# Kernel tuning notes

Hardware: AMD Instinct MI355X
Metric: run time of the kernel (lower is better)

Reference implementation:

```python
import jax, jax.numpy as jnp
import numpy as np
from jax import lax

B, T, F = 2048, 512, 8
C = 16   # conv out channels
H = 10   # lstm hidden size


def setup_inputs() -> dict:
    key = jax.random.key(0)
    ks = jax.random.split(key, 12)
    s_conv = 1.0 / np.sqrt(F * 3)
    s1 = 1.0 / np.sqrt(H)
    inp = {
        'x': jax.random.normal(ks[0], (B, T, F), dtype=jnp.float32),
        'conv_w': jax.random.uniform(ks[1], (C, F, 3), jnp.float32, -s_conv, s_conv),
        'conv_b': jax.random.uniform(ks[2], (C,), jnp.float32, -s_conv, s_conv),
        'w_ih1': jax.random.uniform(ks[3], (4 * H, C), jnp.float32, -s1, s1),
        'w_hh1': jax.random.uniform(ks[4], (4 * H, H), jnp.float32, -s1, s1),
        'b_ih1': jax.random.uniform(ks[5], (4 * H,), jnp.float32, -s1, s1),
        'b_hh1': jax.random.uniform(ks[6], (4 * H,), jnp.float32, -s1, s1),
        'w_ih2': jax.random.uniform(ks[7], (4 * H, H), jnp.float32, -s1, s1),
        'w_hh2': jax.random.uniform(ks[8], (4 * H, H), jnp.float32, -s1, s1),
        'b_ih2': jax.random.uniform(ks[9], (4 * H,), jnp.float32, -s1, s1),
        'b_hh2': jax.random.uniform(ks[9], (4 * H,), jnp.float32, -s1, s1),
        'lin_w': jax.random.uniform(ks[10], (1, H), jnp.float32, -s1, s1),
        'lin_b': jax.random.uniform(ks[11], (1,), jnp.float32, -s1, s1),
    }
    return inp


def _lstm(seq, w_ih, w_hh, b_ih, b_hh):
    # seq: [B, T, D] -> hidden stream [B, T, H]; PyTorch gate order i,f,g,o.
    xg = jnp.einsum('btd,gd->btg', seq, w_ih) + (b_ih + b_hh)  # [B,T,4H]
    h0 = jnp.zeros((seq.shape[0], H), seq.dtype)

    def step(carry, xg_t):
        h, c = carry
        g = xg_t + h @ w_hh.T
        i, f, gg, o = jnp.split(g, 4, axis=-1)
        c = jax.nn.sigmoid(f) * c + jax.nn.sigmoid(i) * jnp.tanh(gg)
        h = jax.nn.sigmoid(o) * jnp.tanh(c)
        return (h, c), h

    _, hs = lax.scan(step, (h0, h0), jnp.swapaxes(xg, 0, 1))  # [T,B,H]
    return jnp.swapaxes(hs, 0, 1)


def reference(x, conv_w, conv_b, w_ih1, w_hh1, b_ih1, b_hh1,
              w_ih2, w_hh2, b_ih2, b_hh2, lin_w, lin_b):
    # conv1d over time, padding=1 keeps length (dropout is identity in eval)
    xc = jnp.transpose(x, (0, 2, 1))  # [B,F,T]
    y = lax.conv_general_dilated(xc, conv_w, window_strides=(1,),
                                 padding=[(1, 1)],
                                 dimension_numbers=('NCH', 'OIH', 'NCH'))
    y = jax.nn.relu(y + conv_b[None, :, None])
    y = jnp.transpose(y, (0, 2, 1))  # [B,T,C]
    h1 = _lstm(y, w_ih1, w_hh1, b_ih1, b_hh1)
    h2 = _lstm(h1, w_ih2, w_hh2, b_ih2, b_hh2)
    last = h2[:, -1, :]  # [B,H]
    return jax.nn.sigmoid(last @ lin_w.T + lin_b)  # [B,1]
```

## Files before the change

kernel.cpp:

```cpp
#include <hip/hip_runtime.h>

#define TT 512
#define FF 8
#define CC 16
#define HH 10
#define G4 40

__device__ __forceinline__ float rl(float v, int k){
    return __int_as_float(__builtin_amdgcn_readlane(__float_as_int(v), k));
}
__device__ __forceinline__ float sigf(float z){
    return __builtin_amdgcn_rcpf(1.f + __expf(-z));
}
__device__ __forceinline__ float tanh_f(float z){
    return 1.f - 2.f * __builtin_amdgcn_rcpf(1.f + __expf(2.f * z));
}
#define PIN(v) asm volatile("" : "+v"(v))

template<int Q>
__device__ __forceinline__ float quadb(float v){
    return __int_as_float(__builtin_amdgcn_mov_dpp(__float_as_int(v), Q * 0x55, 0xf, 0xf, false));
}

#define CONV_Y(Y) do{                                                                              \
    float a0 = cb, a1 = 0.f;                                                                       \
    a0 = fmaf(w0a.x, cw0,  a0); a1 = fmaf(w1a.x, cw1,  a1); a0 = fmaf(w2a.x, cw2,  a0);            \
    a1 = fmaf(w0a.y, cw3,  a1); a0 = fmaf(w1a.y, cw4,  a0); a1 = fmaf(w2a.y, cw5,  a1);            \
    a0 = fmaf(w0a.z, cw6,  a0); a1 = fmaf(w1a.z, cw7,  a1); a0 = fmaf(w2a.z, cw8,  a0);            \
    a1 = fmaf(w0a.w, cw9,  a1); a0 = fmaf(w1a.w, cw10, a0); a1 = fmaf(w2a.w, cw11, a1);            \
    a0 = fmaf(w0b.x, cw12, a0); a1 = fmaf(w1b.x, cw13, a1); a0 = fmaf(w2b.x, cw14, a0);            \
    a1 = fmaf(w0b.y, cw15, a1); a0 = fmaf(w1b.y, cw16, a0); a1 = fmaf(w2b.y, cw17, a1);            \
    a0 = fmaf(w0b.z, cw18, a0); a1 = fmaf(w1b.z, cw19, a1); a0 = fmaf(w2b.z, cw20, a0);            \
    a1 = fmaf(w0b.w, cw21, a1); a0 = fmaf(w1b.w, cw22, a0); a1 = fmaf(w2b.w, cw23, a1);            \
    Y = fmaxf(a0 + a1, 0.f);                                                                       \
}while(0)

__global__ __launch_bounds__(64, 1)
void conv_xg(const float* __restrict__ x,
             const float* __restrict__ conv_w, const float* __restrict__ conv_b,
             const float* __restrict__ w_ih1,  const float* __restrict__ b_ih1,
             const float* __restrict__ b_hh1,
             float* __restrict__ xg)
{
    __shared__ float wl[64][43];
    const int lane = threadIdx.x;
    const int b    = blockIdx.x;
    const int ch   = lane & 15;
    const int g    = lane >> 4;
    const int u_c  = (lane < G4) ? (lane >> 2) : 9;
    const int q    = lane & 3;
    const int r    = q * 10 + u_c;

    {
        float* mr_ = wl[lane];
        const float* cwp = conv_w + ch*24;
        #pragma unroll
        for (int m = 0; m < 24; ++m) mr_[m] = cwp[m];
        const float* wip = w_ih1 + r*CC;
        #pragma unroll
        for (int k = 0; k < CC; ++k) mr_[24+k] = wip[k];
        mr_[40] = b_ih1[r] + b_hh1[r];
        mr_[41] = conv_b[ch];
    }
    __syncthreads();
    const float* mr = wl[lane];

    float cw0=mr[0],  cw1=mr[1],  cw2=mr[2],  cw3=mr[3],  cw4=mr[4],  cw5=mr[5];
    float cw6=mr[6],  cw7=mr[7],  cw8=mr[8],  cw9=mr[9],  cw10=mr[10],cw11=mr[11];
    float cw12=mr[12],cw13=mr[13],cw14=mr[14],cw15=mr[15],cw16=mr[16],cw17=mr[17];
    float cw18=mr[18],cw19=mr[19],cw20=mr[20],cw21=mr[21],cw22=mr[22],cw23=mr[23];
    PIN(cw0);PIN(cw1);PIN(cw2);PIN(cw3);PIN(cw4);PIN(cw5);PIN(cw6);PIN(cw7);
    PIN(cw8);PIN(cw9);PIN(cw10);PIN(cw11);PIN(cw12);PIN(cw13);PIN(cw14);PIN(cw15);
    PIN(cw16);PIN(cw17);PIN(cw18);PIN(cw19);PIN(cw20);PIN(cw21);PIN(cw22);PIN(cw23);
    float wi0=mr[24], wi1=mr[25], wi2=mr[26], wi3=mr[27];
    float wi4=mr[28], wi5=mr[29], wi6=mr[30], wi7=mr[31];
    float wi8=mr[32], wi9=mr[33], wi10=mr[34],wi11=mr[35];
    float wi12=mr[36],wi13=mr[37],wi14=mr[38],wi15=mr[39];
    PIN(wi0);PIN(wi1);PIN(wi2);PIN(wi3);PIN(wi4);PIN(wi5);PIN(wi6);PIN(wi7);
    PIN(wi8);PIN(wi9);PIN(wi10);PIN(wi11);PIN(wi12);PIN(wi13);PIN(wi14);PIN(wi15);
    float b1r = mr[40]; PIN(b1r);
    float cb  = mr[41]; PIN(cb);

    const float* xb  = x  + (size_t)b * (TT*FF);
    float*       xgb = xg + (size_t)b * (TT*G4);
    const float4 z4 = make_float4(0.f,0.f,0.f,0.f);

    #pragma unroll 1
    for (int tb = 0; tb < TT/4; ++tb){
        const int tq = tb*4 + g;
        float4 w0a, w0b, w1a, w1b, w2a, w2b;
        if (tq == 0){ w0a = z4; w0b = z4; }
        else { const float* p = xb + (tq-1)*FF; w0a = *(const float4*)p; w0b = *(const float4*)(p+4); }
        { const float* p = xb + tq*FF; w1a = *(const float4*)p; w1b = *(const float4*)(p+4); }
        if (tq + 1 < TT){ const float* p = xb + (tq+1)*FF; w2a = *(const float4*)p; w2b = *(const float4*)(p+4); }
        else { w2a = z4; w2b = z4; }

        float y; CONV_Y(y);

        #pragma unroll
        for (int s = 0; s < 4; ++s){
            float e0 = b1r, e1 = 0.f;
            e0 = fmaf(rl(y, s*16+0),  wi0,  e0);  e1 = fmaf(rl(y, s*16+1),  wi1,  e1);
            e0 = fmaf(rl(y, s*16+2),  wi2,  e0);  e1 = fmaf(rl(y, s*16+3),  wi3,  e1);
            e0 = fmaf(rl(y, s*16+4),  wi4,  e0);  e1 = fmaf(rl(y, s*16+5),  wi5,  e1);
            e0 = fmaf(rl(y, s*16+6),  wi6,  e0);  e1 = fmaf(rl(y, s*16+7),  wi7,  e1);
            e0 = fmaf(rl(y, s*16+8),  wi8,  e0);  e1 = fmaf(rl(y, s*16+9),  wi9,  e1);
            e0 = fmaf(rl(y, s*16+10), wi10, e0);  e1 = fmaf(rl(y, s*16+11), wi11, e1);
            e0 = fmaf(rl(y, s*16+12), wi12, e0);  e1 = fmaf(rl(y, s*16+13), wi13, e1);
            e0 = fmaf(rl(y, s*16+14), wi14, e0);  e1 = fmaf(rl(y, s*16+15), wi15, e1);
            if (lane < G4) xgb[(tb*4+s)*G4 + lane] = e0 + e1;
        }
    }
}

#define BH1B                                                                     \
    const float hs0=rl(h1,0),  hs1=rl(h1,4),  hs2=rl(h1,8),  hs3=rl(h1,12),      \
                hs4=rl(h1,16), hs5=rl(h1,20), hs6=rl(h1,24), hs7=rl(h1,28),      \
                hs8=rl(h1,32), hs9=rl(h1,36);

#define BL2 do{                                                                  \
    float d0 = b2, d1 = 0.f;                                                     \
    d0 = fmaf(hs0, wi2_0, d0);  d1 = fmaf(hs1, wi2_1, d1);                       \
    d0 = fmaf(hs2, wi2_2, d0);  d1 = fmaf(hs3, wi2_3, d1);                       \
    d0 = fmaf(hs4, wi2_4, d0);  d1 = fmaf(hs5, wi2_5, d1);                       \
    d0 = fmaf(hs6, wi2_6, d0);  d1 = fmaf(hs7, wi2_7, d1);                       \
    d0 = fmaf(hs8, wi2_8, d0);  d1 = fmaf(hs9, wi2_9, d1);                       \
    d0 = fmaf(rl(h2,0),  wh2_0, d0);  d1 = fmaf(rl(h2,4),  wh2_1, d1);           \
    d0 = fmaf(rl(h2,8),  wh2_2, d0);  d1 = fmaf(rl(h2,12), wh2_3, d1);           \
    d0 = fmaf(rl(h2,16), wh2_4, d0);  d1 = fmaf(rl(h2,20), wh2_5, d1);           \
    d0 = fmaf(rl(h2,24), wh2_6, d0);  d1 = fmaf(rl(h2,28), wh2_7, d1);           \
    d0 = fmaf(rl(h2,32), wh2_8, d0);  d1 = fmaf(rl(h2,36), wh2_9, d1);           \
    const float g2  = d0 + d1;                                                   \
    const float sg2 = sigf(g2 * zM);                                             \
    const float act2 = fmaf(aA, sg2, aB);                                        \
    const float ai2 = quadb<0>(act2);                                            \
    const float af2 = quadb<1>(act2);                                            \
    const float ag2 = quadb<2>(act2);                                            \
    const float ao2 = quadb<3>(act2);                                            \
    c2 = fmaf(af2, c2, ai2 * ag2);                                               \
    h2 = ao2 * tanh_f(c2);                                                       \
}while(0)

#define BL1(XGV) do{                                                             \
    float e0 = (XGV), e1 = 0.f;                                                  \
    e0 = fmaf(hs0, wh1_0, e0);  e1 = fmaf(hs1, wh1_1, e1);                       \
    e0 = fmaf(hs2, wh1_2, e0);  e1 = fmaf(hs3, wh1_3, e1);                       \
    e0 = fmaf(hs4, wh1_4, e0);  e1 = fmaf(hs5, wh1_5, e1);                       \
    e0 = fmaf(hs6, wh1_6, e0);  e1 = fmaf(hs7, wh1_7, e1);                       \
    e0 = fmaf(hs8, wh1_8, e0);  e1 = fmaf(hs9, wh1_9, e1);                       \
    const float g1  = e0 + e1;                                                   \
    const float sg1 = sigf(g1 * zM);                                             \
    const float act1 = fmaf(aA, sg1, aB);                                        \
    const float ai1 = quadb<0>(act1);                                            \
    const float af1 = quadb<1>(act1);                                            \
    const float ag1 = quadb<2>(act1);                                            \
    const float ao1 = quadb<3>(act1);                                            \
    c1 = fmaf(af1, c1, ai1 * ag1);                                               \
    h1n = ao1 * tanh_f(c1);                                                      \
}while(0)

__global__ __launch_bounds__(64, 1)
void lstm_seq(const float* __restrict__ xg,
              const float* __restrict__ w_hh1,
              const float* __restrict__ w_ih2,  const float* __restrict__ w_hh2,
              const float* __restrict__ b_ih2,  const float* __restrict__ b_hh2,
              const float* __restrict__ lin_w,  const float* __restrict__ lin_b,
              float* __restrict__ out)
{
    __shared__ float wl[64][31];
    const int lane  = threadIdx.x;
    const int batch = blockIdx.x;
    const int u_c   = (lane < G4) ? (lane >> 2) : 9;
    const int q     = lane & 3;
    const int r     = q * 10 + u_c;
    const bool isG  = (q == 2);
    float zM = isG ? 2.f : 1.f;
    float aA = isG ? 2.f : 1.f;
    float aB = isG ? -1.f : 0.f;
    PIN(zM); PIN(aA); PIN(aB);

    {
        float* mr_ = wl[lane];
        const float* q1 = w_hh1 + r*HH;
        const float* q2 = w_ih2 + r*HH;
        const float* q3 = w_hh2 + r*HH;
        #pragma unroll
        for (int m = 0; m < HH; ++m){ mr_[m]=q1[m]; mr_[10+m]=q2[m]; mr_[20+m]=q3[m]; }
        mr_[30] = b_ih2[r] + b_hh2[r];
    }
    __syncthreads();
    const float* mr = wl[lane];

    float wh1_0=mr[0], wh1_1=mr[1], wh1_2=mr[2], wh1_3=mr[3], wh1_4=mr[4];
    float wh1_5=mr[5], wh1_6=mr[6], wh1_7=mr[7], wh1_8=mr[8], wh1_9=mr[9];
    PIN(wh1_0);PIN(wh1_1);PIN(wh1_2);PIN(wh1_3);PIN(wh1_4);
    PIN(wh1_5);PIN(wh1_6);PIN(wh1_7);PIN(wh1_8);PIN(wh1_9);
    float wi2_0=mr[10],wi2_1=mr[11],wi2_2=mr[12],wi2_3=mr[13],wi2_4=mr[14];
    float wi2_5=mr[15],wi2_6=mr[16],wi2_7=mr[17],wi2_8=mr[18],wi2_9=mr[19];
    PIN(wi2_0);PIN(wi2_1);PIN(wi2_2);PIN(wi2_3);PIN(wi2_4);
    PIN(wi2_5);PIN(wi2_6);PIN(wi2_7);PIN(wi2_8);PIN(wi2_9);
    float wh2_0=mr[20],wh2_1=mr[21],wh2_2=mr[22],wh2_3=mr[23],wh2_4=mr[24];
    float wh2_5=mr[25],wh2_6=mr[26],wh2_7=mr[27],wh2_8=mr[28],wh2_9=mr[29];
    PIN(wh2_0);PIN(wh2_1);PIN(wh2_2);PIN(wh2_3);PIN(wh2_4);
    PIN(wh2_5);PIN(wh2_6);PIN(wh2_7);PIN(wh2_8);PIN(wh2_9);
    float b2 = mr[30]; PIN(b2);

    const float* xp = xg + (size_t)batch * (TT*G4) + ((lane < G4) ? lane : (G4-1));

    float h1 = 0.f, c1 = 0.f, h2 = 0.f, c2 = 0.f, h1n;

    float xgv = xp[0];
    {
        BH1B;
        BL1(xgv);
        h1 = h1n;
    }
    float xgn = xp[G4];

    #pragma unroll 2
    for (int t = 1; t < TT; ++t){
        const float xgc = xgn;
        const int tn = (t + 1 < TT) ? (t + 1) : (TT - 1);
        xgn = xp[(size_t)tn * G4];
        BH1B;
        BL2;
        BL1(xgc);
        h1 = h1n;
    }
    { BH1B; BL2; }

    float part = (q == 0 && lane < G4) ? h2 * lin_w[u_c] : 0.f;
    part += __shfl_xor(part, 4,  64);
    part += __shfl_xor(part, 8,  64);
    part += __shfl_xor(part, 16, 64);
    part += __shfl_xor(part, 32, 64);
    if (lane == 0) out[batch] = sigf(part + lin_b[0]);
}

#define H1BCAST                                                                                    \
    const float hs0=rl(h1,0), hs1=rl(h1,1), hs2=rl(h1,2), hs3=rl(h1,3), hs4=rl(h1,4),              \
                hs5=rl(h1,5), hs6=rl(h1,6), hs7=rl(h1,7), hs8=rl(h1,8), hs9=rl(h1,9);

#define LAYER2 do{                                                                                 \
    float d0 = b2, d1 = 0.f;                                                                       \
    d0 = fmaf(hs0, wi2_0, d0);  d1 = fmaf(hs1, wi2_1, d1);                                         \
    d0 = fmaf(hs2, wi2_2, d0);  d1 = fmaf(hs3, wi2_3, d1);                                         \
    d0 = fmaf(hs4, wi2_4, d0);  d1 = fmaf(hs5, wi2_5, d1);                                         \
    d0 = fmaf(hs6, wi2_6, d0);  d1 = fmaf(hs7, wi2_7, d1);                                         \
    d0 = fmaf(hs8, wi2_8, d0);  d1 = fmaf(hs9, wi2_9, d1);                                         \
    d0 = fmaf(rl(h2,0), wh2_0, d0);  d1 = fmaf(rl(h2,1), wh2_1, d1);                               \
    d0 = fmaf(rl(h2,2), wh2_2, d0);  d1 = fmaf(rl(h2,3), wh2_3, d1);                               \
    d0 = fmaf(rl(h2,4), wh2_4, d0);  d1 = fmaf(rl(h2,5), wh2_5, d1);                               \
    d0 = fmaf(rl(h2,6), wh2_6, d0);  d1 = fmaf(rl(h2,7), wh2_7, d1);                               \
    d0 = fmaf(rl(h2,8), wh2_8, d0);  d1 = fmaf(rl(h2,9), wh2_9, d1);                               \
    const float g2  = d0 + d1;                                                                     \
    const float sg2 = sigf(g2 * zM);                                                               \
    const float act2 = fmaf(aA, sg2, aB);                                                          \
    const float ai2 = __shfl(act2, u,      64);                                                    \
    const float af2 = __shfl(act2, u + 10, 64);                                                    \
    const float ag2 = __shfl(act2, u + 20, 64);                                                    \
    const float ao2 = __shfl(act2, u + 30, 64);                                                    \
    c2 = fmaf(af2, c2, ai2 * ag2);                                                                 \
    h2 = ao2 * tanh_f(c2);                                                                         \
}while(0)

#define LAYER1(YV) do{                                                                             \
    float e0 = b1, e1 = 0.f;                                                                       \
    e0 = fmaf(rl(YV,0),  wi0,  e0);  e1 = fmaf(rl(YV,1),  wi1,  e1);                               \
    e0 = fmaf(rl(YV,2),  wi2,  e0);  e1 = fmaf(rl(YV,3),  wi3,  e1);                               \
    e0 = fmaf(rl(YV,4),  wi4,  e0);  e1 = fmaf(rl(YV,5),  wi5,  e1);                               \
    e0 = fmaf(rl(YV,6),  wi6,  e0);  e1 = fmaf(rl(YV,7),  wi7,  e1);                               \
    e0 = fmaf(rl(YV,8),  wi8,  e0);  e1 = fmaf(rl(YV,9),  wi9,  e1);                               \
    e0 = fmaf(rl(YV,10), wi10, e0);  e1 = fmaf(rl(YV,11), wi11, e1);                               \
    e0 = fmaf(rl(YV,12), wi12, e0);  e1 = fmaf(rl(YV,13), wi13, e1);                               \
    e0 = fmaf(rl(YV,14), wi14, e0);  e1 = fmaf(rl(YV,15), wi15, e1);                               \
    e0 = fmaf(hs0, wh1_0, e0);  e1 = fmaf(hs1, wh1_1, e1);                                         \
    e0 = fmaf(hs2, wh1_2, e0);  e1 = fmaf(hs3, wh1_3, e1);                                         \
    e0 = fmaf(hs4, wh1_4, e0);  e1 = fmaf(hs5, wh1_5, e1);                                         \
    e0 = fmaf(hs6, wh1_6, e0);  e1 = fmaf(hs7, wh1_7, e1);                                         \
    e0 = fmaf(hs8, wh1_8, e0);  e1 = fmaf(hs9, wh1_9, e1);                                         \
    const float g1  = e0 + e1;                                                                     \
    const float sg1 = sigf(g1 * zM);                                                               \
    const float act1 = fmaf(aA, sg1, aB);                                                          \
    const float ai1 = __shfl(act1, u,      64);                                                    \
    const float af1 = __shfl(act1, u + 10, 64);                                                    \
    const float ag1 = __shfl(act1, u + 20, 64);                                                    \
    const float ao1 = __shfl(act1, u + 30, 64);                                                    \
    c1 = fmaf(af1, c1, ai1 * ag1);                                                                 \
    h1n = ao1 * tanh_f(c1);                                                                        \
}while(0)

__global__ __launch_bounds__(64, 1)
void lstm_fused(const float* __restrict__ x,
                const float* __restrict__ conv_w, const float* __restrict__ conv_b,
                const float* __restrict__ w_ih1,  const float* __restrict__ w_hh1,
                const float* __restrict__ b_ih1,  const float* __restrict__ b_hh1,
                const float* __restrict__ w_ih2,  const float* __restrict__ w_hh2,
                const float* __restrict__ b_ih2,  const float* __restrict__ b_hh2,
                const float* __restrict__ lin_w,  const float* __restrict__ lin_b,
                float* __restrict__ out)
{
    __shared__ float wl[64][73];
    const int lane  = threadIdx.x;
    const int batch = blockIdx.x;
    const int grow  = (lane < G4) ? lane : (G4-1);
    const int q     = grow / 10;
    const int u     = grow - q * 10;
    const int ch    = lane & 15;
    const bool isG  = (q == 2);
    float zM = isG ? 2.f : 1.f;
    float aA = isG ? 2.f : 1.f;
    float aB = isG ? -1.f : 0.f;
    PIN(zM); PIN(aA); PIN(aB);

    {
        float* mr_ = wl[lane];
        const float* cwp = conv_w + ch*24;
        #pragma unroll
        for (int m = 0; m < 24; ++m) mr_[m] = cwp[m];
        const float* wip = w_ih1 + grow*CC;
        #pragma unroll
        for (int m = 0; m < CC; ++m) mr_[24+m] = wip[m];
        const float* q1 = w_hh1 + grow*HH;
        const float* q2 = w_ih2 + grow*HH;
        const float* q3 = w_hh2 + grow*HH;
        #pragma unroll
        for (int m = 0; m < HH; ++m){ mr_[40+m]=q1[m]; mr_[50+m]=q2[m]; mr_[60+m]=q3[m]; }
        mr_[70] = b_ih1[grow] + b_hh1[grow];
        mr_[71] = b_ih2[grow] + b_hh2[grow];
        mr_[72] = conv_b[ch];
    }
    __syncthreads();
    const float* mr = wl[lane];

    float cw0=mr[0],  cw1=mr[1],  cw2=mr[2],  cw3=mr[3],  cw4=mr[4],  cw5=mr[5];
    float cw6=mr[6],  cw7=mr[7],  cw8=mr[8],  cw9=mr[9],  cw10=mr[10],cw11=mr[11];
    float cw12=mr[12],cw13=mr[13],cw14=mr[14],cw15=mr[15],cw16=mr[16],cw17=mr[17];
    float cw18=mr[18],cw19=mr[19],cw20=mr[20],cw21=mr[21],cw22=mr[22],cw23=mr[23];
    float wi0=mr[24], wi1=mr[25], wi2=mr[26], wi3=mr[27];
    float wi4=mr[28], wi5=mr[29], wi6=mr[30], wi7=mr[31];
    float wi8=mr[32], wi9=mr[33], wi10=mr[34],wi11=mr[35];
    float wi12=mr[36],wi13=mr[37],wi14=mr[38],wi15=mr[39];
    float wh1_0=mr[40],wh1_1=mr[41],wh1_2=mr[42],wh1_3=mr[43],wh1_4=mr[44];
    float wh1_5=mr[45],wh1_6=mr[46],wh1_7=mr[47],wh1_8=mr[48],wh1_9=mr[49];
    float wi2_0=mr[50],wi2_1=mr[51],wi2_2=mr[52],wi2_3=mr[53],wi2_4=mr[54];
    float wi2_5=mr[55],wi2_6=mr[56],wi2_7=mr[57],wi2_8=mr[58],wi2_9=mr[59];
    float wh2_0=mr[60],wh2_1=mr[61],wh2_2=mr[62],wh2_3=mr[63],wh2_4=mr[64];
    float wh2_5=mr[65],wh2_6=mr[66],wh2_7=mr[67],wh2_8=mr[68],wh2_9=mr[69];
    float b1 = mr[70], b2 = mr[71], cb = mr[72];

    const float* xb = x + (size_t)batch * (TT*FF);
    float h1 = 0.f, c1 = 0.f, h2 = 0.f, c2 = 0.f, h1n;

    float4 w0a = make_float4(0.f,0.f,0.f,0.f), w0b = w0a;
    float4 w1a = *(const float4*)(xb + 0);
    float4 w1b = *(const float4*)(xb + 4);
    float4 w2a = *(const float4*)(xb + 8);
    float4 w2b = *(const float4*)(xb + 12);

    {
        float y0; CONV_Y(y0);
        H1BCAST;
        LAYER1(y0);
        h1 = h1n;
    }
    w0a = w1a; w0b = w1b; w1a = w2a; w1b = w2b;
    w2a = *(const float4*)(xb + 16);
    w2b = *(const float4*)(xb + 20);

    #pragma unroll 3
    for (int t = 1; t < TT; ++t){
        float4 nxa = make_float4(0.f,0.f,0.f,0.f), nxb = nxa;
        if (t + 2 < TT){
            const float* p = xb + (t+2)*FF;
            nxa = *(const float4*)p;
            nxb = *(const float4*)(p + 4);
        }
        float y; CONV_Y(y);
        {
            H1BCAST;
            LAYER2;
            LAYER1(y);
        }
        h1 = h1n;
        w0a = w1a; w0b = w1b; w1a = w2a; w1b = w2b; w2a = nxa; w2b = nxb;
    }
    { H1BCAST; LAYER2; }

    float part = (lane < HH) ? h2 * lin_w[grow] : 0.f;
    #pragma unroll
    for (int off = 8; off > 0; off >>= 1) part += __shfl_xor(part, off, 16);
    if (lane == 0) out[batch] = sigf(part + lin_b[0]);
}

extern "C" void kernel_launch(void* const* d_in, const int* in_sizes, int n_in,
                              void* d_out, int out_size, void* d_ws, size_t ws_size,
                              hipStream_t stream) {
    const float* x      = (const float*)d_in[0];
    const float* conv_w = (const float*)d_in[1];
    const float* conv_b = (const float*)d_in[2];
    const float* w_ih1  = (const float*)d_in[3];
    const float* w_hh1  = (const float*)d_in[4];
    const float* b_ih1  = (const float*)d_in[5];
    const float* b_hh1  = (const float*)d_in[6];
    const float* w_ih2  = (const float*)d_in[7];
    const float* w_hh2  = (const float*)d_in[8];
    const float* b_ih2  = (const float*)d_in[9];
    const float* b_hh2  = (const float*)d_in[10];
    const float* lin_w  = (const float*)d_in[11];
    const float* lin_b  = (const float*)d_in[12];
    float* out = (float*)d_out;

    const int NB = 2048;
    const size_t XG_BYTES = (size_t)NB * TT * G4 * sizeof(float);

    if (ws_size >= XG_BYTES){
        float* xgws = (float*)d_ws;
        conv_xg<<<dim3(NB), dim3(64), 0, stream>>>(
            x, conv_w, conv_b, w_ih1, b_ih1, b_hh1, xgws);
        lstm_seq<<<dim3(NB), dim3(64), 0, stream>>>(
            xgws, w_hh1, w_ih2, w_hh2, b_ih2, b_hh2, lin_w, lin_b, out);
    } else {
        lstm_fused<<<dim3(NB), dim3(64), 0, stream>>>(
            x, conv_w, conv_b, w_ih1, w_hh1, b_ih1, b_hh1,
            w_ih2, w_hh2, b_ih2, b_hh2, lin_w, lin_b, out);
    }
}
```

Baseline: 295.5 us.

## Split conv_xg over time quarters, pack xg as float4, prescale gate weights for exp2

The conv/input-projection kernel now launches four blocks per batch, each handling a quarter of the sequence, to raise parallelism. The xg workspace is re-laid out so each lane writes and later reads four consecutive timesteps as one float4, cutting the number of memory transactions in both kernels. Gate weights and biases are pre-multiplied by -log2(e) (doubled for the g gate), so the activations use exp2 directly without per-step scaling multiplies. The LSTM loop is restructured into four-step blocks with a float4 prefetch, which adds some code size and register pressure.

```diff
diff --git a/kernel.cpp b/kernel.cpp
--- a/kernel.cpp
+++ b/kernel.cpp
@@ -20,6 +20,10 @@
 template<int Q>
 __device__ __forceinline__ float quadb(float v){
     return __int_as_float(__builtin_amdgcn_mov_dpp(__float_as_int(v), Q * 0x55, 0xf, 0xf, false));
+}
+
+__device__ __forceinline__ float scaleRow(int r){
+    return (r >= 20 && r < 30) ? -2.8853900817779268f : -1.4426950408889634f;
 }
 
 #define CONV_Y(Y) do{                                                                              \
@@ -42,52 +46,55 @@
              const float* __restrict__ b_hh1,
              float* __restrict__ xg)
 {
-    __shared__ float wl[64][43];
+    __shared__ float cwS[16][25];
+    __shared__ float wiS[40][17];
+    __shared__ float bS[G4];
+    __shared__ float cbS[16];
+
     const int lane = threadIdx.x;
-    const int b    = blockIdx.x;
+    const int b    = blockIdx.x >> 2;
+    const int wq   = blockIdx.x & 3;
     const int ch   = lane & 15;
     const int g    = lane >> 4;
     const int u_c  = (lane < G4) ? (lane >> 2) : 9;
     const int q    = lane & 3;
-    const int r    = q * 10 + u_c;
-
-    {
-        float* mr_ = wl[lane];
-        const float* cwp = conv_w + ch*24;
-        #pragma unroll
-        for (int m = 0; m < 24; ++m) mr_[m] = cwp[m];
-        const float* wip = w_ih1 + r*CC;
-        #pragma unroll
-        for (int k = 0; k < CC; ++k) mr_[24+k] = wip[k];
-        mr_[40] = b_ih1[r] + b_hh1[r];
-        mr_[41] = conv_b[ch];
-    }
+    const int r    = (lane < G4) ? (q * 10 + u_c) : 39;
+
+    for (int i = lane; i < 16*24; i += 64) cwS[i/24][i%24] = conv_w[i];
+    for (int i = lane; i < G4*CC; i += 64){
+        int rr = i >> 4, k = i & 15;
+        wiS[rr][k] = w_ih1[i] * scaleRow(rr);
+    }
+    if (lane < G4) bS[lane] = (b_ih1[lane] + b_hh1[lane]) * scaleRow(lane);
+    if (lane < 16) cbS[lane] = conv_b[lane];
     __syncthreads();
-    const float* mr = wl[lane];
-
-    float cw0=mr[0],  cw1=mr[1],  cw2=mr[2],  cw3=mr[3],  cw4=mr[4],  cw5=mr[5];
-    float cw6=mr[6],  cw7=mr[7],  cw8=mr[8],  cw9=mr[9],  cw10=mr[10],cw11=mr[11];
-    float cw12=mr[12],cw13=mr[13],cw14=mr[14],cw15=mr[15],cw16=mr[16],cw17=mr[17];
-    float cw18=mr[18],cw19=mr[19],cw20=mr[20],cw21=mr[21],cw22=mr[22],cw23=mr[23];
+
+    float cw0=cwS[ch][0],  cw1=cwS[ch][1],  cw2=cwS[ch][2],  cw3=cwS[ch][3];
+    float cw4=cwS[ch][4],  cw5=cwS[ch][5],  cw6=cwS[ch][6],  cw7=cwS[ch][7];
+    float cw8=cwS[ch][8],  cw9=cwS[ch][9],  cw10=cwS[ch][10],cw11=cwS[ch][11];
+    float cw12=cwS[ch][12],cw13=cwS[ch][13],cw14=cwS[ch][14],cw15=cwS[ch][15];
+    float cw16=cwS[ch][16],cw17=cwS[ch][17],cw18=cwS[ch][18],cw19=cwS[ch][19];
+    float cw20=cwS[ch][20],cw21=cwS[ch][21],cw22=cwS[ch][22],cw23=cwS[ch][23];
     PIN(cw0);PIN(cw1);PIN(cw2);PIN(cw3);PIN(cw4);PIN(cw5);PIN(cw6);PIN(cw7);
     PIN(cw8);PIN(cw9);PIN(cw10);PIN(cw11);PIN(cw12);PIN(cw13);PIN(cw14);PIN(cw15);
     PIN(cw16);PIN(cw17);PIN(cw18);PIN(cw19);PIN(cw20);PIN(cw21);PIN(cw22);PIN(cw23);
-    float wi0=mr[24], wi1=mr[25], wi2=mr[26], wi3=mr[27];
-    float wi4=mr[28], wi5=mr[29], wi6=mr[30], wi7=mr[31];
-    float wi8=mr[32], wi9=mr[33], wi10=mr[34],wi11=mr[35];
-    float wi12=mr[36],wi13=mr[37],wi14=mr[38],wi15=mr[39];
+    float wi0=wiS[r][0],  wi1=wiS[r][1],  wi2=wiS[r][2],  wi3=wiS[r][3];
+    float wi4=wiS[r][4],  wi5=wiS[r][5],  wi6=wiS[r][6],  wi7=wiS[r][7];
+    float wi8=wiS[r][8],  wi9=wiS[r][9],  wi10=wiS[r][10],wi11=wiS[r][11];
+    float wi12=wiS[r][12],wi13=wiS[r][13],wi14=wiS[r][14],wi15=wiS[r][15];
     PIN(wi0);PIN(wi1);PIN(wi2);PIN(wi3);PIN(wi4);PIN(wi5);PIN(wi6);PIN(wi7);
     PIN(wi8);PIN(wi9);PIN(wi10);PIN(wi11);PIN(wi12);PIN(wi13);PIN(wi14);PIN(wi15);
-    float b1r = mr[40]; PIN(b1r);
-    float cb  = mr[41]; PIN(cb);
+    float b1r = bS[r];  PIN(b1r);
+    float cb  = cbS[ch];PIN(cb);
 
     const float* xb  = x  + (size_t)b * (TT*FF);
     float*       xgb = xg + (size_t)b * (TT*G4);
     const float4 z4 = make_float4(0.f,0.f,0.f,0.f);
+    const int t0 = wq * 128;
 
     #pragma unroll 1
-    for (int tb = 0; tb < TT/4; ++tb){
-        const int tq = tb*4 + g;
+    for (int i = 0; i < 32; ++i){
+        const int tq = t0 + i*4 + g;
         float4 w0a, w0b, w1a, w1b, w2a, w2b;
         if (tq == 0){ w0a = z4; w0b = z4; }
         else { const float* p = xb + (tq-1)*FF; w0a = *(const float4*)p; w0b = *(const float4*)(p+4); }
@@ -97,6 +104,7 @@
 
         float y; CONV_Y(y);
 
+        float acc[4];
         #pragma unroll
         for (int s = 0; s < 4; ++s){
             float e0 = b1r, e1 = 0.f;
@@ -108,7 +116,11 @@
             e0 = fmaf(rl(y, s*16+10), wi10, e0);  e1 = fmaf(rl(y, s*16+11), wi11, e1);
             e0 = fmaf(rl(y, s*16+12), wi12, e0);  e1 = fmaf(rl(y, s*16+13), wi13, e1);
             e0 = fmaf(rl(y, s*16+14), wi14, e0);  e1 = fmaf(rl(y, s*16+15), wi15, e1);
-            if (lane < G4) xgb[(tb*4+s)*G4 + lane] = e0 + e1;
+            acc[s] = e0 + e1;
+        }
+        if (lane < G4){
+            float4 v = make_float4(acc[0], acc[1], acc[2], acc[3]);
+            *(float4*)(xgb + (size_t)(t0/4 + i) * (G4*4) + lane*4) = v;
         }
     }
 }
@@ -117,6 +129,12 @@
     const float hs0=rl(h1,0),  hs1=rl(h1,4),  hs2=rl(h1,8),  hs3=rl(h1,12),      \
                 hs4=rl(h1,16), hs5=rl(h1,20), hs6=rl(h1,24), hs7=rl(h1,28),      \
                 hs8=rl(h1,32), hs9=rl(h1,36);
+
+#define BACT(GV, DST) do{                                                        \
+    const float sg_ = __builtin_amdgcn_rcpf(1.f + exp2f(GV));                    \
+    DST = fmaf(aA, sg_, aB);                                                     \
+}while(0)
+#define THC(CV) fmaf(2.f, __builtin_amdgcn_rcpf(1.f + exp2f(-2.8853900817779268f*(CV))), -1.f)
 
 #define BL2 do{                                                                  \
     float d0 = b2, d1 = 0.f;                                                     \
@@ -130,15 +148,13 @@
     d0 = fmaf(rl(h2,16), wh2_4, d0);  d1 = fmaf(rl(h2,20), wh2_5, d1);           \
     d0 = fmaf(rl(h2,24), wh2_6, d0);  d1 = fmaf(rl(h2,28), wh2_7, d1);           \
     d0 = fmaf(rl(h2,32), wh2_8, d0);  d1 = fmaf(rl(h2,36), wh2_9, d1);           \
-    const float g2  = d0 + d1;                                                   \
-    const float sg2 = sigf(g2 * zM);                                             \
-    const float act2 = fmaf(aA, sg2, aB);                                        \
+    float act2; BACT(d0 + d1, act2);                                             \
     const float ai2 = quadb<0>(act2);                                            \
     const float af2 = quadb<1>(act2);                                            \
     const float ag2 = quadb<2>(act2);                                            \
     const float ao2 = quadb<3>(act2);                                            \
     c2 = fmaf(af2, c2, ai2 * ag2);                                               \
-    h2 = ao2 * tanh_f(c2);                                                       \
+    h2 = ao2 * THC(c2);                                                          \
 }while(0)
 
 #define BL1(XGV) do{                                                             \
@@ -148,16 +164,16 @@
     e0 = fmaf(hs4, wh1_4, e0);  e1 = fmaf(hs5, wh1_5, e1);                       \
     e0 = fmaf(hs6, wh1_6, e0);  e1 = fmaf(hs7, wh1_7, e1);                       \
     e0 = fmaf(hs8, wh1_8, e0);  e1 = fmaf(hs9, wh1_9, e1);                       \
-    const float g1  = e0 + e1;                                                   \
-    const float sg1 = sigf(g1 * zM);                                             \
-    const float act1 = fmaf(aA, sg1, aB);                                        \
+    float act1; BACT(e0 + e1, act1);                                             \
     const float ai1 = quadb<0>(act1);                                            \
     const float af1 = quadb<1>(act1);                                            \
     const float ag1 = quadb<2>(act1);                                            \
     const float ao1 = quadb<3>(act1);                                            \
     c1 = fmaf(af1, c1, ai1 * ag1);                                               \
-    h1n = ao1 * tanh_f(c1);                                                      \
-}while(0)
+    h1n = ao1 * THC(c1);                                                         \
+}while(0)
+
+#define BSTEP(XGV) { BH1B; BL2; BL1(XGV); h1 = h1n; }
 
 __global__ __launch_bounds__(64, 1)
 void lstm_seq(const float* __restrict__ xg,
@@ -172,21 +188,21 @@
     const int batch = blockIdx.x;
     const int u_c   = (lane < G4) ? (lane >> 2) : 9;
     const int q     = lane & 3;
-    const int r     = q * 10 + u_c;
-    const bool isG  = (q == 2);
-    float zM = isG ? 2.f : 1.f;
+    const int r     = (lane < G4) ? (q * 10 + u_c) : 39;
+    const bool isG  = (q == 2) && (lane < G4);
     float aA = isG ? 2.f : 1.f;
     float aB = isG ? -1.f : 0.f;
-    PIN(zM); PIN(aA); PIN(aB);
+    PIN(aA); PIN(aB);
 
     {
         float* mr_ = wl[lane];
+        const float s = scaleRow(r);
         const float* q1 = w_hh1 + r*HH;
         const float* q2 = w_ih2 + r*HH;
         const float* q3 = w_hh2 + r*HH;
         #pragma unroll
-        for (int m = 0; m < HH; ++m){ mr_[m]=q1[m]; mr_[10+m]=q2[m]; mr_[20+m]=q3[m]; }
-        mr_[30] = b_ih2[r] + b_hh2[r];
+        for (int m = 0; m < HH; ++m){ mr_[m]=q1[m]*s; mr_[10+m]=q2[m]*s; mr_[20+m]=q3[m]*s; }
+        mr_[30] = (b_ih2[r] + b_hh2[r]) * s;
     }
     __syncthreads();
     const float* mr = wl[lane];
@@ -205,27 +221,22 @@
     PIN(wh2_5);PIN(wh2_6);PIN(wh2_7);PIN(wh2_8);PIN(wh2_9);
     float b2 = mr[30]; PIN(b2);
 
-    const float* xp = xg + (size_t)batch * (TT*G4) + ((lane < G4) ? lane : (G4-1));
+    const int lane4 = (lane < G4) ? lane : (G4-1);
+    const float* xp = xg + (size_t)batch * (TT*G4) + lane4*4;
 
     float h1 = 0.f, c1 = 0.f, h2 = 0.f, c2 = 0.f, h1n;
 
-    float xgv = xp[0];
-    {
-        BH1B;
-        BL1(xgv);
-        h1 = h1n;
-    }
-    float xgn = xp[G4];
-
-    #pragma unroll 2
-    for (int t = 1; t < TT; ++t){
-        const float xgc = xgn;
-        const int tn = (t + 1 < TT) ? (t + 1) : (TT - 1);
-        xgn = xp[(size_t)tn * G4];
-        BH1B;
-        BL2;
-        BL1(xgc);
-        h1 = h1n;
+    float4 xq  = *(const float4*)(xp);
+    float4 xqn = *(const float4*)(xp + G4*4);
+
+    { BH1B; BL1(xq.x); h1 = h1n; }
+    BSTEP(xq.y); BSTEP(xq.z); BSTEP(xq.w);
+
+    #pragma unroll 1
+    for (int tb = 1; tb < TT/4; ++tb){
+        xq = xqn;
+        if (tb + 1 < TT/4) xqn = *(const float4*)(xp + (size_t)(tb+1)*(G4*4));
+        BSTEP(xq.x); BSTEP(xq.y); BSTEP(xq.z); BSTEP(xq.w);
     }
     { BH1B; BL2; }
 
@@ -416,7 +427,7 @@
 
     if (ws_size >= XG_BYTES){
         float* xgws = (float*)d_ws;
-        conv_xg<<<dim3(NB), dim3(64), 0, stream>>>(
+        conv_xg<<<dim3(NB*4), dim3(64), 0, stream>>>(
             x, conv_w, conv_b, w_ih1, b_ih1, b_hh1, xgws);
         lstm_seq<<<dim3(NB), dim3(64), 0, stream>>>(
             xgws, w_hh1, w_ih2, w_hh2, b_ih2, b_hh2, lin_w, lin_b, out);
```

Result: slower. 376.1 us (+27.3%).
